# Optimization experiments

Hardware: AMD Instinct MI355X
Metric: run time of the kernel (lower is better)

## Reference

```python
import jax, jax.numpy as jnp
import numpy as np

WH, WW = 16, 16          # window size
NUM_HEADS = 6
DIM = 192
N = WH * WW              # tokens per window

def _rel_coords_table():
    # (2*WH-1, 2*WW-1, 2), normalized and scaled by 8 (Swin-V2 style)
    rch = np.arange(-(WH - 1), WH, dtype=np.float32)
    rcw = np.arange(-(WW - 1), WW, dtype=np.float32)
    tab = np.stack(np.meshgrid(rch, rcw, indexing='ij'), axis=-1)
    tab[..., 0] /= (WH - 1)
    tab[..., 1] /= (WW - 1)
    tab *= 8.0
    return tab

def _rel_pos_index():
    # (N, N) int indices into the flattened bias table
    coords = np.stack(np.meshgrid(np.arange(WH), np.arange(WW), indexing='ij'))  # (2,WH,WW)
    cf = coords.reshape(2, -1)                                                   # (2,N)
    rel = cf[:, :, None] - cf[:, None, :]                                        # (2,N,N)
    rel = rel.transpose(1, 2, 0).astype(np.int64)                                # (N,N,2)
    rel[..., 0] += WH - 1
    rel[..., 1] += WW - 1
    rel[..., 0] *= 2 * WW - 1
    return rel.sum(-1)                                                           # (N,N)

_TABLE = jnp.asarray(_rel_coords_table())          # (2WH-1, 2WW-1, 2)
_INDEX = jnp.asarray(_rel_pos_index().reshape(-1)) # (N*N,)

def setup_inputs() -> dict:
    key = jax.random.key(0)
    ks = jax.random.split(key, 8)
    B_ = 256  # num_windows(64) * batch(4)
    return {
        'x': jax.random.normal(ks[0], (B_, N, DIM), dtype=jnp.float32),
        'scale': jax.random.uniform(ks[1], (1, 2), dtype=jnp.float32),
        'mask': jnp.zeros((64, N, N), dtype=jnp.float32),
        'qkv_w': jax.random.normal(ks[2], (3 * DIM, DIM), dtype=jnp.float32) * 0.02,
        'qkv_b': jnp.zeros((3 * DIM,), dtype=jnp.float32),
        'cpb_w1': jax.random.normal(ks[3], (512, 4), dtype=jnp.float32) * 0.02,
        'cpb_b1': jnp.zeros((512,), dtype=jnp.float32),
        'cpb_w2': jax.random.normal(ks[4], (NUM_HEADS, 512), dtype=jnp.float32) * 0.02,
        'cpb_b2': jnp.zeros((NUM_HEADS,), dtype=jnp.float32),
        'proj_w': jax.random.normal(ks[5], (DIM, DIM), dtype=jnp.float32) * 0.02,
        'proj_b': jnp.zeros((DIM,), dtype=jnp.float32),
    }

def reference(x, scale, mask, qkv_w, qkv_b, cpb_w1, cpb_b1, cpb_w2, cpb_b2, proj_w, proj_b):
    B_, n, C = x.shape
    H = NUM_HEADS
    hd = C // H
    qk_scale = hd ** -0.5

    qkv = x @ qkv_w.T + qkv_b                       # (B_, N, 3C)
    qkv = qkv.reshape(B_, n, 3, H, hd).transpose(2, 0, 3, 1, 4)
    q, k, v = qkv[0], qkv[1], qkv[2]                # each (B_, H, N, hd)

    attn = jnp.einsum('bhnd,bhmd->bhnm', q * qk_scale, k)  # (B_, H, N, N)

    # continuous relative position bias: concat table with broadcast scale -> MLP
    rel_cell = jnp.broadcast_to(scale[0], _TABLE.shape[:2] + (2,))    # (2WH-1,2WW-1,2)
    coords4 = jnp.concatenate([_TABLE, rel_cell], axis=-1)            # (...,4)
    hmid = jax.nn.relu(coords4 @ cpb_w1.T + cpb_b1)                   # (...,512)
    table = (hmid @ cpb_w2.T + cpb_b2).reshape(-1, H)                 # (M, H)
    bias = table[_INDEX].reshape(n, n, H).transpose(2, 0, 1)          # (H, N, N)

    attn = attn + bias[None]
    nW = mask.shape[0]
    attn = attn.reshape(B_ // nW, nW, H, n, n) + mask[None, :, None]
    attn = attn.reshape(B_, H, n, n)
    attn = jax.nn.softmax(attn, axis=-1)

    out = jnp.einsum('bhnm,bhmd->bhnd', attn, v)    # (B_, H, N, hd)
    out = out.transpose(0, 2, 1, 3).reshape(B_, n, C)
    return out @ proj_w.T + proj_b
```

## Files before the change

### kernel.cpp

```cpp
#include <hip/hip_runtime.h>
#include <math.h>

#define N_TOK 256
#define NHEADS 6
#define DIM_C 192
#define HD 32
#define B_WIN 256

typedef short bf16x8 __attribute__((ext_vector_type(8)));
typedef float f32x4 __attribute__((ext_vector_type(4)));

__device__ inline short f2bf(float f) {
    unsigned u = __float_as_uint(f);
    u = (u + 0x7fffu + ((u >> 16) & 1u)) >> 16;
    return (short)u;
}
__device__ inline short f2bf_fast(float f) {
    return (short)((__float_as_uint(f) + 0x8000u) >> 16);
}
__device__ inline float bf2f(short s) {
    return __uint_as_float(((unsigned)(unsigned short)s) << 16);
}

__global__ __launch_bounds__(512) void cpb_table_kernel(
    const float* __restrict__ scale, const float* __restrict__ w1,
    const float* __restrict__ b1, const float* __restrict__ w2,
    const float* __restrict__ b2, float* __restrict__ table)
{
    __shared__ float red[512];
    const int e = blockIdx.x;
    const int i = e / 31, j = e % 31;
    const float t0 = ((float)(i - 15)) * (8.0f / 15.0f);
    const float t1 = ((float)(j - 15)) * (8.0f / 15.0f);
    const float s0 = scale[0], s1 = scale[1];
    const int t = threadIdx.x;
    const float* w = w1 + t * 4;
    float h = w[0] * t0 + w[1] * t1 + w[2] * s0 + w[3] * s1 + b1[t];
    h = fmaxf(h, 0.0f);
    for (int head = 0; head < NHEADS; ++head) {
        red[t] = h * w2[head * 512 + t];
        __syncthreads();
        for (int s = 256; s > 0; s >>= 1) {
            if (t < s) red[t] += red[t + s];
            __syncthreads();
        }
        if (t == 0) table[e * NHEADS + head] = red[0] + b2[head];
        __syncthreads();
    }
}


__global__ __launch_bounds__(256) void bias_perm_kernel(
    const float* __restrict__ table, short* __restrict__ bias_p)
{
    const int idx8 = blockIdx.x * 256 + threadIdx.x;
    const int h = idx8 >> 13;
    const int rem = idx8 & 8191;
    const int rb = rem >> 9;
    const int g = (rem >> 6) & 7;
    const int lane = rem & 63;
    const int quad = lane >> 4, l15 = lane & 15;
    bf16x8 o;
#pragma unroll
    for (int j = 0; j < 8; ++j) {
        const int nt = g * 2 + (j >> 2), r = j & 3;
        const int row = rb * 16 + quad * 4 + r;
        const int col = nt * 16 + l15;
        const int rel0 = (row >> 4) - (col >> 4) + 15;
        const int rel1 = (row & 15) - (col & 15) + 15;
        o[j] = f2bf(table[(rel0 * 31 + rel1) * NHEADS + h]);
    }
    ((bf16x8*)bias_p)[idx8] = o;
}

__global__ __launch_bounds__(256) void mask_perm_kernel(
    const float* __restrict__ mask, short* __restrict__ mask_p)
{
    const int idx8 = blockIdx.x * 256 + threadIdx.x;
    const int bw = idx8 >> 13;
    const int rem = idx8 & 8191;
    const int rb = rem >> 9;
    const int g = (rem >> 6) & 7;
    const int lane = rem & 63;
    const int quad = lane >> 4, l15 = lane & 15;
    const float* ms = mask + ((size_t)bw << 16);
    bf16x8 o;
#pragma unroll
    for (int j = 0; j < 8; ++j) {
        const int nt = g * 2 + (j >> 2), r = j & 3;
        const int row = rb * 16 + quad * 4 + r;
        const int col = nt * 16 + l15;
        o[j] = f2bf(ms[row * 256 + col]);
    }
    ((bf16x8*)mask_p)[idx8] = o;
}

__global__ __launch_bounds__(256) void f32_to_bf16_kernel(
    const float* __restrict__ in, short* __restrict__ out, int n4)
{
    const int i = blockIdx.x * 256 + threadIdx.x;
    if (i < n4) {
        float4 v = ((const float4*)in)[i];
        short4 s;
        s.x = f2bf(v.x); s.y = f2bf(v.y); s.z = f2bf(v.z); s.w = f2bf(v.w);
        ((short4*)out)[i] = s;
    }
}

__global__ __launch_bounds__(256) void qkv_gemm_kernel(
    const short* __restrict__ x16, const short* __restrict__ w16,
    const float* __restrict__ qkv_b,
    short* __restrict__ qb, short* __restrict__ kb, short* __restrict__ vb)
{
    const int t = threadIdx.x;
    const int lane = t & 63;
    const int w = t >> 6;
    const int l15 = lane & 15, quad = lane >> 4;

    const int l = blockIdx.x;
    const int xcd = l & 7;
    const int s = l >> 3;
    const int cb = s % 6;
    const int panel = xcd + 8 * (s / 6);
    const int m0 = panel * 128 + w * 32;
    const int n0 = cb * 96;

    bf16x8 af[2][6];
#pragma unroll
    for (int mt = 0; mt < 2; ++mt)
#pragma unroll
        for (int ks = 0; ks < 6; ++ks)
            af[mt][ks] = *(const bf16x8*)(x16 + (size_t)(m0 + mt * 16 + l15) * DIM_C + ks * 32 + quad * 8);

    bf16x8 wb[2][6];
#pragma unroll
    for (int c4 = 0; c4 < 6; ++c4)
        wb[0][c4] = *(const bf16x8*)(w16 + (size_t)(n0 + c4 * 16 + l15) * DIM_C + quad * 8);

    f32x4 acc[2][6] = {};
#pragma unroll
    for (int ks = 0; ks < 6; ++ks) {
        if (ks < 5) {
#pragma unroll
            for (int c4 = 0; c4 < 6; ++c4)
                wb[(ks + 1) & 1][c4] = *(const bf16x8*)(w16 + (size_t)(n0 + c4 * 16 + l15) * DIM_C + (ks + 1) * 32 + quad * 8);
        }
#pragma unroll
        for (int mt = 0; mt < 2; ++mt)
#pragma unroll
            for (int c4 = 0; c4 < 6; ++c4)
                acc[mt][c4] = __builtin_amdgcn_mfma_f32_16x16x32_bf16(af[mt][ks], wb[ks & 1][c4], acc[mt][c4], 0, 0, 0);
    }

    const int which = cb >> 1;
    short* outp = (which == 0) ? qb : (which == 1) ? kb : vb;
    const float qscale = (which == 0) ? 0.17677669529663689f : 1.0f;
#pragma unroll
    for (int mt = 0; mt < 2; ++mt) {
#pragma unroll
        for (int r = 0; r < 4; ++r) {
            const int m = m0 + mt * 16 + quad * 4 + r;
            const int b = m >> 8, tok = m & 255;
#pragma unroll
            for (int c4 = 0; c4 < 6; ++c4) {
                const int rem = (cb & 1) * 96 + c4 * 16 + l15;
                const int h = rem >> 5, d = rem & 31;
                const float val = (acc[mt][c4][r] + qkv_b[which * DIM_C + rem]) * qscale;
                outp[((size_t)((b * NHEADS + h) * N_TOK + tok)) * HD + d] = f2bf(val);
            }
        }
    }
}

__global__ __launch_bounds__(256) void proj_gemm_kernel(
    const short* __restrict__ A16, const short* __restrict__ w16,
    const float* __restrict__ proj_b, float* __restrict__ out)
{
    const int t = threadIdx.x;
    const int lane = t & 63;
    const int w = t >> 6;
    const int l15 = lane & 15, quad = lane >> 4;

    const int l = blockIdx.x;
    const int xcd = l & 7;
    const int s = l >> 3;
    const int cb = s % 2;
    const int panel = xcd + 8 * (s / 2);
    const int m0 = panel * 128 + w * 32;
    const int n0 = cb * 96;

    bf16x8 af[2][6];
#pragma unroll
    for (int mt = 0; mt < 2; ++mt)
#pragma unroll
        for (int ks = 0; ks < 6; ++ks)
            af[mt][ks] = *(const bf16x8*)(A16 + (size_t)(m0 + mt * 16 + l15) * DIM_C + ks * 32 + quad * 8);

    bf16x8 wb[2][6];
#pragma unroll
    for (int c4 = 0; c4 < 6; ++c4)
        wb[0][c4] = *(const bf16x8*)(w16 + (size_t)(n0 + c4 * 16 + l15) * DIM_C + quad * 8);

    f32x4 acc[2][6] = {};
#pragma unroll
    for (int ks = 0; ks < 6; ++ks) {
        if (ks < 5) {
#pragma unroll
            for (int c4 = 0; c4 < 6; ++c4)
                wb[(ks + 1) & 1][c4] = *(const bf16x8*)(w16 + (size_t)(n0 + c4 * 16 + l15) * DIM_C + (ks + 1) * 32 + quad * 8);
        }
#pragma unroll
        for (int mt = 0; mt < 2; ++mt)
#pragma unroll
            for (int c4 = 0; c4 < 6; ++c4)
                acc[mt][c4] = __builtin_amdgcn_mfma_f32_16x16x32_bf16(af[mt][ks], wb[ks & 1][c4], acc[mt][c4], 0, 0, 0);
    }

#pragma unroll
    for (int mt = 0; mt < 2; ++mt) {
#pragma unroll
        for (int r = 0; r < 4; ++r) {
            const int m = m0 + mt * 16 + quad * 4 + r;
#pragma unroll
            for (int c4 = 0; c4 < 6; ++c4) {
                const int c = n0 + c4 * 16 + l15;
                out[(size_t)m * DIM_C + c] = acc[mt][c4][r] + proj_b[c];
            }
        }
    }
}

#define PS_LD 264

__global__ __launch_bounds__(256, 3) void attn_mfma_kernel(
    const short* __restrict__ q, const short* __restrict__ k,
    const short* __restrict__ v, const short* __restrict__ bias_p,
    const short* __restrict__ mask_p, short* __restrict__ out16)
{
    __shared__ __align__(16) short Vt[32][PS_LD];
    __shared__ __align__(16) short Pw[4][16][PS_LD];

    const int l = blockIdx.x;
    const int s = l >> 3;
    const int bw = (l & 7) + 8 * (s / 24);
    const int j = s % 24;
    const int h = j % 6;
    const int b = (j / 6) * 64 + bw;

    const int t = threadIdx.x;
    const int lane = t & 63;
    const int w = t >> 6;
    const int l15 = lane & 15;
    const int quad = lane >> 4;
    const size_t slab = ((size_t)(b * NHEADS + h)) * (N_TOK * HD);

    {
        const bf16x8* vrow = (const bf16x8*)(v + slab + (size_t)t * HD);
#pragma unroll
        for (int u = 0; u < 4; ++u) {
            bf16x8 vv = vrow[u];
#pragma unroll
            for (int jj = 0; jj < 8; ++jj) {
                const int d = u * 8 + jj;
                Vt[d][t ^ (((d >> 3) & 1) * 16)] = vv[jj];
            }
        }
    }

    bf16x8 kfr[16];
#pragma unroll
    for (int nt = 0; nt < 16; ++nt)
        kfr[nt] = *(const bf16x8*)(k + slab + (size_t)(nt * 16 + l15) * HD + quad * 8);

    __syncthreads();

    const short* bslab = bias_p + h * 65536;
    const short* mslab = mask_p + bw * 65536;

    for (int chunk = 0; chunk < 4; ++chunk) {
        const int rb = chunk * 4 + w;

        const bf16x8 qf = *(const bf16x8*)(q + slab + (size_t)(rb * 16 + l15) * HD + quad * 8);

        f32x4 S[16];
#pragma unroll
        for (int half = 0; half < 2; ++half) {
            bf16x8 bb[4], mm[4];
#pragma unroll
            for (int gg = 0; gg < 4; ++gg) {
                const int g = half * 4 + gg;
                const int off = ((rb * 8 + g) * 64 + lane) * 8;
                bb[gg] = *(const bf16x8*)(bslab + off);
                mm[gg] = *(const bf16x8*)(mslab + off);
            }
#pragma unroll
            for (int gg = 0; gg < 4; ++gg) {
                const int g = half * 4 + gg;
                f32x4 c0, c1;
#pragma unroll
                for (int r = 0; r < 4; ++r) {
                    c0[r] = bf2f(bb[gg][r])     + bf2f(mm[gg][r]);
                    c1[r] = bf2f(bb[gg][4 + r]) + bf2f(mm[gg][4 + r]);
                }
                S[g * 2]     = __builtin_amdgcn_mfma_f32_16x16x32_bf16(qf, kfr[g * 2],     c0, 0, 0, 0);
                S[g * 2 + 1] = __builtin_amdgcn_mfma_f32_16x16x32_bf16(qf, kfr[g * 2 + 1], c1, 0, 0, 0);
            }
        }

        float mx[4] = {-1e30f, -1e30f, -1e30f, -1e30f};
#pragma unroll
        for (int nt = 0; nt < 16; ++nt)
#pragma unroll
            for (int r = 0; r < 4; ++r)
                mx[r] = fmaxf(mx[r], S[nt][r]);
#pragma unroll
        for (int r = 0; r < 4; ++r) {
            mx[r] = fmaxf(mx[r], __shfl_xor(mx[r], 1));
            mx[r] = fmaxf(mx[r], __shfl_xor(mx[r], 2));
            mx[r] = fmaxf(mx[r], __shfl_xor(mx[r], 4));
            mx[r] = fmaxf(mx[r], __shfl_xor(mx[r], 8));
        }

        float sm[4] = {0.f, 0.f, 0.f, 0.f};
#pragma unroll
        for (int nt = 0; nt < 16; ++nt) {
#pragma unroll
            for (int r = 0; r < 4; ++r) {
                const float p = __expf(S[nt][r] - mx[r]);
                sm[r] += p;
                const int lr = quad * 4 + r;
                Pw[w][lr][(nt * 16 + l15) ^ (((lr >> 3) & 1) * 16)] = f2bf_fast(p);
            }
        }
        float inv[4];
#pragma unroll
        for (int r = 0; r < 4; ++r) {
            sm[r] += __shfl_xor(sm[r], 1);
            sm[r] += __shfl_xor(sm[r], 2);
            sm[r] += __shfl_xor(sm[r], 4);
            sm[r] += __shfl_xor(sm[r], 8);
            inv[r] = __builtin_amdgcn_rcpf(sm[r]);
        }

        __asm__ volatile("s_waitcnt lgkmcnt(0)" ::: "memory");

        f32x4 O0 = {0.f, 0.f, 0.f, 0.f};
        f32x4 O1 = {0.f, 0.f, 0.f, 0.f};
        const int sw = ((l15 >> 3) & 1) * 16;
#pragma unroll
        for (int ks = 0; ks < 8; ++ks) {
            const int cb = ks * 32 + quad * 8;
            bf16x8 af  = *(const bf16x8*)&Pw[w][l15][cb ^ sw];
            bf16x8 bf0 = *(const bf16x8*)&Vt[l15][cb ^ sw];
            bf16x8 bf1 = *(const bf16x8*)&Vt[16 + l15][cb ^ sw];
            O0 = __builtin_amdgcn_mfma_f32_16x16x32_bf16(af, bf0, O0, 0, 0, 0);
            O1 = __builtin_amdgcn_mfma_f32_16x16x32_bf16(af, bf1, O1, 0, 0, 0);
        }

#pragma unroll
        for (int r = 0; r < 4; ++r) {
            const int token = rb * 16 + quad * 4 + r;
            short* dst = out16 + ((size_t)(b * N_TOK + token)) * DIM_C + h * HD;
            dst[l15]      = f2bf_fast(O0[r] * inv[r]);
            dst[16 + l15] = f2bf_fast(O1[r] * inv[r]);
        }
    }
}

extern "C" void kernel_launch(void* const* d_in, const int* in_sizes, int n_in,
                              void* d_out, int out_size, void* d_ws, size_t ws_size,
                              hipStream_t stream)
{
    const float* x      = (const float*)d_in[0];
    const float* scale  = (const float*)d_in[1];
    const float* mask   = (const float*)d_in[2];
    const float* qkv_w  = (const float*)d_in[3];
    const float* qkv_b  = (const float*)d_in[4];
    const float* cpb_w1 = (const float*)d_in[5];
    const float* cpb_b1 = (const float*)d_in[6];
    const float* cpb_w2 = (const float*)d_in[7];
    const float* cpb_b2 = (const float*)d_in[8];
    const float* proj_w = (const float*)d_in[9];
    const float* proj_b = (const float*)d_in[10];
    float* out = (float*)d_out;

    const size_t per = (size_t)B_WIN * NHEADS * N_TOK * HD;
    short* wss     = (short*)d_ws;
    short* qb      = wss;
    short* kb      = qb + per;
    short* vb      = kb + per;
    short* ao      = vb + per;
    short* x16     = ao + per;
    short* bias_p  = x16 + per;
    short* mask_p  = bias_p + 393216;
    short* qkvw16  = mask_p + 4194304;
    short* projw16 = qkvw16 + 110592;
    float* table   = (float*)(projw16 + 36864);

    cpb_table_kernel<<<961, 512, 0, stream>>>(scale, cpb_w1, cpb_b1, cpb_w2, cpb_b2, table);

    bias_perm_kernel<<<(NHEADS * 8192) / 256, 256, 0, stream>>>(table, bias_p);
    mask_perm_kernel<<<(64 * 8192) / 256, 256, 0, stream>>>(mask, mask_p);

    f32_to_bf16_kernel<<<(int)((per / 4 + 255) / 256), 256, 0, stream>>>(x, x16, (int)(per / 4));
    f32_to_bf16_kernel<<<(110592 / 4 + 255) / 256, 256, 0, stream>>>(qkv_w, qkvw16, 110592 / 4);
    f32_to_bf16_kernel<<<(36864 / 4 + 255) / 256, 256, 0, stream>>>(proj_w, projw16, 36864 / 4);

    qkv_gemm_kernel<<<3072, 256, 0, stream>>>(x16, qkvw16, qkv_b, qb, kb, vb);

    attn_mfma_kernel<<<NHEADS * B_WIN, 256, 0, stream>>>(qb, kb, vb, bias_p, mask_p, ao);

    proj_gemm_kernel<<<1024, 256, 0, stream>>>(ao, projw16, proj_b, out);
}
```

Before: 318.4 us.

## Compute transposed S tile so softmax reductions stay mostly in-lane

```diff
diff --git a/kernel.cpp b/kernel.cpp
--- a/kernel.cpp
+++ b/kernel.cpp
@@ -20,6 +20,11 @@
 }
 __device__ inline float bf2f(short s) {
     return __uint_as_float(((unsigned)(unsigned short)s) << 16);
+}
+__device__ inline unsigned cvt_pk_bf16(float lo, float hi) {
+    unsigned r;
+    asm("v_cvt_pk_bf16_f32 %0, %1, %2" : "=v"(r) : "v"(lo), "v"(hi));
+    return r;
 }
 
 __global__ __launch_bounds__(512) void cpb_table_kernel(
@@ -64,10 +69,8 @@
 #pragma unroll
     for (int j = 0; j < 8; ++j) {
         const int nt = g * 2 + (j >> 2), r = j & 3;
-        const int row = rb * 16 + quad * 4 + r;
-        const int col = nt * 16 + l15;
-        const int rel0 = (row >> 4) - (col >> 4) + 15;
-        const int rel1 = (row & 15) - (col & 15) + 15;
+        const int rel0 = rb - nt + 15;
+        const int rel1 = l15 - (quad * 4 + r) + 15;
         o[j] = f2bf(table[(rel0 * 31 + rel1) * NHEADS + h]);
     }
     ((bf16x8*)bias_p)[idx8] = o;
@@ -88,9 +91,9 @@
 #pragma unroll
     for (int j = 0; j < 8; ++j) {
         const int nt = g * 2 + (j >> 2), r = j & 3;
-        const int row = rb * 16 + quad * 4 + r;
-        const int col = nt * 16 + l15;
-        o[j] = f2bf(ms[row * 256 + col]);
+        const int q = rb * 16 + l15;
+        const int k = nt * 16 + quad * 4 + r;
+        o[j] = f2bf(ms[q * 256 + k]);
     }
     ((bf16x8*)mask_p)[idx8] = o;
 }
@@ -276,6 +279,7 @@
 
     const short* bslab = bias_p + h * 65536;
     const short* mslab = mask_p + bw * 65536;
+    const int sw = ((l15 >> 3) & 1) * 16;
 
     for (int chunk = 0; chunk < 4; ++chunk) {
         const int rb = chunk * 4 + w;
@@ -302,51 +306,44 @@
                     c0[r] = bf2f(bb[gg][r])     + bf2f(mm[gg][r]);
                     c1[r] = bf2f(bb[gg][4 + r]) + bf2f(mm[gg][4 + r]);
                 }
-                S[g * 2]     = __builtin_amdgcn_mfma_f32_16x16x32_bf16(qf, kfr[g * 2],     c0, 0, 0, 0);
-                S[g * 2 + 1] = __builtin_amdgcn_mfma_f32_16x16x32_bf16(qf, kfr[g * 2 + 1], c1, 0, 0, 0);
+                S[g * 2]     = __builtin_amdgcn_mfma_f32_16x16x32_bf16(kfr[g * 2],     qf, c0, 0, 0, 0);
+                S[g * 2 + 1] = __builtin_amdgcn_mfma_f32_16x16x32_bf16(kfr[g * 2 + 1], qf, c1, 0, 0, 0);
             }
         }
 
-        float mx[4] = {-1e30f, -1e30f, -1e30f, -1e30f};
+        float mxp[4] = {-1e30f, -1e30f, -1e30f, -1e30f};
 #pragma unroll
         for (int nt = 0; nt < 16; ++nt)
 #pragma unroll
             for (int r = 0; r < 4; ++r)
-                mx[r] = fmaxf(mx[r], S[nt][r]);
-#pragma unroll
-        for (int r = 0; r < 4; ++r) {
-            mx[r] = fmaxf(mx[r], __shfl_xor(mx[r], 1));
-            mx[r] = fmaxf(mx[r], __shfl_xor(mx[r], 2));
-            mx[r] = fmaxf(mx[r], __shfl_xor(mx[r], 4));
-            mx[r] = fmaxf(mx[r], __shfl_xor(mx[r], 8));
-        }
+                mxp[r] = fmaxf(mxp[r], S[nt][r]);
+        float mx = fmaxf(fmaxf(mxp[0], mxp[1]), fmaxf(mxp[2], mxp[3]));
+        mx = fmaxf(mx, __shfl_xor(mx, 16));
+        mx = fmaxf(mx, __shfl_xor(mx, 32));
 
         float sm[4] = {0.f, 0.f, 0.f, 0.f};
+        short* prow = &Pw[w][l15][0];
 #pragma unroll
         for (int nt = 0; nt < 16; ++nt) {
-#pragma unroll
-            for (int r = 0; r < 4; ++r) {
-                const float p = __expf(S[nt][r] - mx[r]);
-                sm[r] += p;
-                const int lr = quad * 4 + r;
-                Pw[w][lr][(nt * 16 + l15) ^ (((lr >> 3) & 1) * 16)] = f2bf_fast(p);
-            }
-        }
-        float inv[4];
-#pragma unroll
-        for (int r = 0; r < 4; ++r) {
-            sm[r] += __shfl_xor(sm[r], 1);
-            sm[r] += __shfl_xor(sm[r], 2);
-            sm[r] += __shfl_xor(sm[r], 4);
-            sm[r] += __shfl_xor(sm[r], 8);
-            inv[r] = __builtin_amdgcn_rcpf(sm[r]);
-        }
+            const float p0 = __expf(S[nt][0] - mx);
+            const float p1 = __expf(S[nt][1] - mx);
+            const float p2 = __expf(S[nt][2] - mx);
+            const float p3 = __expf(S[nt][3] - mx);
+            sm[0] += p0; sm[1] += p1; sm[2] += p2; sm[3] += p3;
+            uint2 pk;
+            pk.x = cvt_pk_bf16(p0, p1);
+            pk.y = cvt_pk_bf16(p2, p3);
+            *(uint2*)&prow[(nt * 16 + quad * 4) ^ sw] = pk;
+        }
+        float smt = (sm[0] + sm[1]) + (sm[2] + sm[3]);
+        smt += __shfl_xor(smt, 16);
+        smt += __shfl_xor(smt, 32);
+        const float inv = __builtin_amdgcn_rcpf(smt);
 
         __asm__ volatile("s_waitcnt lgkmcnt(0)" ::: "memory");
 
         f32x4 O0 = {0.f, 0.f, 0.f, 0.f};
         f32x4 O1 = {0.f, 0.f, 0.f, 0.f};
-        const int sw = ((l15 >> 3) & 1) * 16;
 #pragma unroll
         for (int ks = 0; ks < 8; ++ks) {
             const int cb = ks * 32 + quad * 8;
@@ -357,12 +354,16 @@
             O1 = __builtin_amdgcn_mfma_f32_16x16x32_bf16(af, bf1, O1, 0, 0, 0);
         }
 
+        float inv_e[4];
+#pragma unroll
+        for (int r = 0; r < 4; ++r)
+            inv_e[r] = __shfl(inv, quad * 4 + r);
 #pragma unroll
         for (int r = 0; r < 4; ++r) {
             const int token = rb * 16 + quad * 4 + r;
             short* dst = out16 + ((size_t)(b * N_TOK + token)) * DIM_C + h * HD;
-            dst[l15]      = f2bf_fast(O0[r] * inv[r]);
-            dst[16 + l15] = f2bf_fast(O1[r] * inv[r]);
+            dst[l15]      = f2bf_fast(O0[r] * inv_e[r]);
+            dst[16 + l15] = f2bf_fast(O1[r] * inv_e[r]);
         }
     }
 }
```

Result: faster. 312.0 us (-2.0%).
